# Kernel tuning notes

Measured on AMD Instinct MI355X. Metric: run time of the kernel, lower is better.

The kernel has to match this reference:

```python
import jax, jax.numpy as jnp
import numpy as np

N_U, N_F = 50000, 20000
N = N_U + N_F
U_DIM, F_DIM, HID = 64, 128, 128
E = 2_000_000        # graph edges
E_PRED = 2_000_000   # prediction pairs
EPS = 1e-5
SLOPE = 0.01         # default leaky_relu negative slope


def setup_inputs() -> dict:
    key = jax.random.key(0)
    ks = jax.random.split(key, 20)
    s = 0.02
    inp = {
        "u_feat": jax.random.normal(ks[0], (N_U, U_DIM), jnp.float32),
        "f_feat": jax.random.normal(ks[1], (N_F, F_DIM), jnp.float32),
        "edge_index": jax.random.randint(ks[2], (2, E), 0, N, jnp.int64),
        "edge_u": jax.random.randint(ks[3], (E_PRED,), 0, N_U, jnp.int64),
        "edge_f": N_U + jax.random.randint(ks[4], (E_PRED,), 0, N_F, jnp.int64),
        # learned params
        "u_W": jax.random.normal(ks[5], (U_DIM, HID), jnp.float32) * s,
        "u_b": jnp.zeros((HID,), jnp.float32),
        "f_W": jax.random.normal(ks[6], (F_DIM, HID), jnp.float32) * s,
        "f_b": jnp.zeros((HID,), jnp.float32),
        "c1_W": jax.random.normal(ks[7], (HID, HID), jnp.float32) * s,
        "c1_b": jnp.zeros((HID,), jnp.float32),
        "c2_W": jax.random.normal(ks[8], (HID, HID), jnp.float32) * s,
        "c2_b": jnp.zeros((HID,), jnp.float32),
        "n1_g": jnp.ones((HID,), jnp.float32),
        "n1_b": jnp.zeros((HID,), jnp.float32),
        "n2_g": jnp.ones((HID,), jnp.float32),
        "n2_b": jnp.zeros((HID,), jnp.float32),
        "e_W": jax.random.normal(ks[9], (2 * HID, 1), jnp.float32) * s,
        "e_b": jnp.zeros((1,), jnp.float32),
        "r_W": jax.random.normal(ks[10], (2 * HID, 1), jnp.float32) * s,
        "r_b": jnp.zeros((1,), jnp.float32),
    }
    return inp


def _layer_norm(x, g, b):
    mu = jnp.mean(x, -1, keepdims=True)
    var = jnp.mean(jnp.square(x - mu), -1, keepdims=True)
    return (x - mu) * jax.lax.rsqrt(var + EPS) * g + b


def _gcn_conv(x, W, b, src, dst, n):
    # PyG GCNConv: add self loops, symmetric deg^{-1/2} norm, aggregate at dst.
    loop = jnp.arange(n, dtype=src.dtype)
    src_f = jnp.concatenate([src, loop])
    dst_f = jnp.concatenate([dst, loop])
    deg = jax.ops.segment_sum(jnp.ones(src_f.shape, x.dtype), dst_f, num_segments=n)
    dinv = jnp.where(deg > 0, jax.lax.rsqrt(deg), 0.0)
    norm = dinv[src_f] * dinv[dst_f]                     # [E+N]
    xw = x @ W                                           # [N, H]
    agg = jax.ops.segment_sum(xw[src_f] * norm[:, None], dst_f, num_segments=n)
    return agg + b


def reference(u_feat, f_feat, edge_index, edge_u, edge_f,
              u_W, u_b, f_W, f_b, c1_W, c1_b, c2_W, c2_b,
              n1_g, n1_b, n2_g, n2_b, e_W, e_b, r_W, r_b):
    src, dst = edge_index[0], edge_index[1]
    x = jnp.concatenate([u_feat @ u_W + u_b, f_feat @ f_W + f_b], 0)  # [N, H]
    x = jax.nn.leaky_relu(_layer_norm(_gcn_conv(x, c1_W, c1_b, src, dst, N), n1_g, n1_b), SLOPE)
    # dropout is identity in eval mode
    x = jax.nn.leaky_relu(_layer_norm(_gcn_conv(x, c2_W, c2_b, src, dst, N), n2_g, n2_b), SLOPE)
    emb = jnp.concatenate([x[edge_u], x[edge_f]], -1)                 # [E_pred, 2H]
    exist = jax.nn.sigmoid((emb @ e_W + e_b)[..., 0])
    rating = 1.0 + 4.0 * jax.nn.sigmoid((emb @ r_W + r_b)[..., 0])
    return exist, rating
```

## Files before the change

### kernel.cpp

```cpp
#include <hip/hip_runtime.h>
#include <hip/hip_bf16.h>
#include <math.h>

#define HID 128
#define SLOPE 0.01f
#define LN_EPS 1e-5f
#define NB_SCAN 256
#define NT_SCAN 256
#define BSHIFT 6
#define CHUNK 8192
#define MAXBUCK 1152

typedef __attribute__((ext_vector_type(8))) short bf16x8;
typedef __attribute__((ext_vector_type(4))) float f32x4;

__device__ __forceinline__ float bf16lo(unsigned int v) {
  unsigned int b = v << 16;
  return __builtin_bit_cast(float, b);
}
__device__ __forceinline__ float bf16hi(unsigned int v) {
  unsigned int b = v & 0xFFFF0000u;
  return __builtin_bit_cast(float, b);
}
__device__ __forceinline__ unsigned int pack_bf16(float lo, float hi) {
  __hip_bfloat16 a = __float2bfloat16(lo);
  __hip_bfloat16 b = __float2bfloat16(hi);
  return (unsigned int)__builtin_bit_cast(unsigned short, a) |
         ((unsigned int)__builtin_bit_cast(unsigned short, b) << 16);
}

__global__ __launch_bounds__(256) void hist_chunk_kernel(
    const int* __restrict__ dst, int* __restrict__ cntM,
    int E, int nbuck, int nchunk) {
  __shared__ int hist[MAXBUCK];
  int c = blockIdx.x, tid = threadIdx.x;
  for (int i = tid; i < nbuck; i += 256) hist[i] = 0;
  __syncthreads();
  int beg = c * CHUNK, end = min(beg + CHUNK, E);
  for (int e = beg + tid; e < end; e += 256)
    atomicAdd(&hist[dst[e] >> BSHIFT], 1);
  __syncthreads();
  for (int b = tid; b < nbuck; b += 256)
    cntM[(size_t)b * nchunk + c] = hist[b];
}

__global__ void scan_pass1(const int* __restrict__ cnt, int* __restrict__ blocksum, int m) {
  __shared__ int ss[NT_SCAN];
  int K = (m + NB_SCAN * NT_SCAN - 1) / (NB_SCAN * NT_SCAN);
  int t = threadIdx.x, b = blockIdx.x;
  int beg = (b * NT_SCAN + t) * K;
  int end = min(beg + K, m);
  int s = 0;
  for (int i = beg; i < end; ++i) s += cnt[i];
  ss[t] = s;
  __syncthreads();
  for (int off = NT_SCAN / 2; off > 0; off >>= 1) {
    if (t < off) ss[t] += ss[t + off];
    __syncthreads();
  }
  if (t == 0) blocksum[b] = ss[0];
}

__global__ void scan_pass2(int* __restrict__ blocksum) {
  __shared__ int ss[NB_SCAN];
  int t = threadIdx.x;
  ss[t] = blocksum[t];
  __syncthreads();
  for (int off = 1; off < NB_SCAN; off <<= 1) {
    int v = (t >= off) ? ss[t - off] : 0;
    __syncthreads();
    ss[t] += v;
    __syncthreads();
  }
  blocksum[t] = (t == 0) ? 0 : ss[t - 1];
}

__global__ void scan_pass3(const int* __restrict__ cnt, const int* __restrict__ blockoff,
                           int* __restrict__ scanM, int m) {
  __shared__ int ss[NT_SCAN];
  int K = (m + NB_SCAN * NT_SCAN - 1) / (NB_SCAN * NT_SCAN);
  int t = threadIdx.x, b = blockIdx.x;
  int beg = (b * NT_SCAN + t) * K;
  int end = min(beg + K, m);
  int s = 0;
  for (int i = beg; i < end; ++i) s += cnt[i];
  ss[t] = s;
  __syncthreads();
  for (int off = 1; off < NT_SCAN; off <<= 1) {
    int v = (t >= off) ? ss[t - off] : 0;
    __syncthreads();
    ss[t] += v;
    __syncthreads();
  }
  int pre = blockoff[b] + ((t == 0) ? 0 : ss[t - 1]);
  for (int i = beg; i < end; ++i) {
    scanM[i] = pre;
    pre += cnt[i];
    if (i == m - 1) scanM[m] = pre;
  }
}

__global__ __launch_bounds__(256) void scatter_chunk_kernel(
    const int* __restrict__ src, const int* __restrict__ dst,
    const int* __restrict__ scanM, unsigned int* __restrict__ ebuf,
    int E, int nbuck, int nchunk) {
  __shared__ int cur[MAXBUCK];
  int c = blockIdx.x, tid = threadIdx.x;
  for (int b = tid; b < nbuck; b += 256)
    cur[b] = scanM[(size_t)b * nchunk + c];
  __syncthreads();
  int beg = c * CHUNK, end = min(beg + CHUNK, E);
  for (int e = beg + tid; e < end; e += 256) {
    int s = src[e], d = dst[e];
    int pos = atomicAdd(&cur[d >> BSHIFT], 1);
    ebuf[pos] = ((unsigned)s << 6) | ((unsigned)d & 63);
  }
}

__global__ __launch_bounds__(256) void deg_rowptr_kernel(
    const unsigned int* __restrict__ ebuf, const int* __restrict__ scanM,
    int* __restrict__ rowptr, float* __restrict__ dinv,
    int n, int nbuck, int nchunk, int E) {
  __shared__ int sdeg[64];
  int b = blockIdx.x, tid = threadIdx.x;
  if (tid < 64) sdeg[tid] = 0;
  __syncthreads();
  int beg = scanM[(size_t)b * nchunk], end = scanM[(size_t)(b + 1) * nchunk];
  for (int j = beg + tid; j < end; j += 256) atomicAdd(&sdeg[ebuf[j] & 63], 1);
  __syncthreads();
  if (tid < 64) {
    int deg = sdeg[tid];
    int s = deg;
#pragma unroll
    for (int off = 1; off < 64; off <<= 1) {
      int v = __shfl_up(s, off);
      if (tid >= off) s += v;
    }
    int excl = s - deg;
    int nd = (b << BSHIFT) + tid;
    if (nd < n) {
      rowptr[nd] = beg + excl;
      dinv[nd] = rsqrtf((float)(deg + 1));
    }
    if (b == nbuck - 1 && tid == 0) rowptr[n] = E;
  }
}

__global__ __launch_bounds__(256) void fill_bucket_kernel(
    const unsigned int* __restrict__ ebuf, const int* __restrict__ scanM,
    const int* __restrict__ rowptr, const float* __restrict__ dinv,
    uint2* __restrict__ ecol, int n, int nchunk) {
  __shared__ int scur[64];
  __shared__ int srow[64];
  __shared__ float sdinv[64];
  int b = blockIdx.x, tid = threadIdx.x;
  if (tid < 64) {
    scur[tid] = 0;
    int nd = (b << BSHIFT) + tid;
    srow[tid] = (nd < n) ? rowptr[nd] : 0;
    sdinv[tid] = (nd < n) ? dinv[nd] : 0.0f;
  }
  __syncthreads();
  int beg = scanM[(size_t)b * nchunk], end = scanM[(size_t)(b + 1) * nchunk];
  for (int j = beg + tid; j < end; j += 256) {
    unsigned int v = ebuf[j];
    int ndl = (int)(v & 63);
    int s = (int)(v >> 6);
    int pos = atomicAdd(&scur[ndl], 1);
    float w = dinv[s] * sdinv[ndl];
    ecol[srow[ndl] + pos] = make_uint2((unsigned)s, __builtin_bit_cast(unsigned int, w));
  }
}

__global__ void wt_pack_kernel(const float* __restrict__ W, unsigned int* __restrict__ Wt,
                               int K) {
  int idx = blockIdx.x * 256 + threadIdx.x;
  int total = 128 * (K / 2);
  if (idx >= total) return;
  int col = idx & 127;
  int k2 = idx >> 7;
  Wt[(size_t)col * (K / 2) + k2] =
      pack_bf16(W[(size_t)(2 * k2) * 128 + col], W[(size_t)(2 * k2 + 1) * 128 + col]);
}

template<int K, bool BF16OUT>
__global__ __launch_bounds__(256) void dense_mfma_kernel(
    const float* __restrict__ feat, const unsigned int* __restrict__ Wt,
    const float* __restrict__ bias,
    float* __restrict__ outf, __hip_bfloat16* __restrict__ outb, int nrows) {
  int tid = threadIdx.x;
  int wid = tid >> 6, lane = tid & 63;
  int l15 = lane & 15, lk = lane >> 4;
  int rowbase = blockIdx.x * 32 + 16 * (wid & 1);
  int colbase = 64 * (wid >> 1);

  f32x4 acc0 = {}, acc1 = {}, acc2 = {}, acc3 = {};

  int row = rowbase + l15;
  int rrow = min(row, nrows - 1);
  const float* ap0 = feat + (size_t)rrow * K + lk * 8;

#pragma unroll
  for (int kb = 0; kb < K / 32; ++kb) {
    const float* ap = ap0 + kb * 32;
    float4 a0 = *reinterpret_cast<const float4*>(ap);
    float4 a1 = *reinterpret_cast<const float4*>(ap + 4);
    float af0 = a0.x, af1 = a0.y, af2 = a0.z, af3 = a0.w;
    float af4 = a1.x, af5 = a1.y, af6 = a1.z, af7 = a1.w;
    unsigned int b0 = __builtin_bit_cast(unsigned int, af0);
    unsigned int b1 = __builtin_bit_cast(unsigned int, af1);
    unsigned int b2 = __builtin_bit_cast(unsigned int, af2);
    unsigned int b3 = __builtin_bit_cast(unsigned int, af3);
    unsigned int b4 = __builtin_bit_cast(unsigned int, af4);
    unsigned int b5 = __builtin_bit_cast(unsigned int, af5);
    unsigned int b6 = __builtin_bit_cast(unsigned int, af6);
    unsigned int b7 = __builtin_bit_cast(unsigned int, af7);
    uint4 hv;
    hv.x = (b0 >> 16) | (b1 & 0xFFFF0000u);
    hv.y = (b2 >> 16) | (b3 & 0xFFFF0000u);
    hv.z = (b4 >> 16) | (b5 & 0xFFFF0000u);
    hv.w = (b6 >> 16) | (b7 & 0xFFFF0000u);
    uint4 lv;
    {
      float h0 = __builtin_bit_cast(float, b0 & 0xFFFF0000u);
      float h1 = __builtin_bit_cast(float, b1 & 0xFFFF0000u);
      float h2 = __builtin_bit_cast(float, b2 & 0xFFFF0000u);
      float h3 = __builtin_bit_cast(float, b3 & 0xFFFF0000u);
      float h4 = __builtin_bit_cast(float, b4 & 0xFFFF0000u);
      float h5 = __builtin_bit_cast(float, b5 & 0xFFFF0000u);
      float h6 = __builtin_bit_cast(float, b6 & 0xFFFF0000u);
      float h7 = __builtin_bit_cast(float, b7 & 0xFFFF0000u);
      lv.x = pack_bf16(af0 - h0, af1 - h1);
      lv.y = pack_bf16(af2 - h2, af3 - h3);
      lv.z = pack_bf16(af4 - h4, af5 - h5);
      lv.w = pack_bf16(af6 - h6, af7 - h7);
    }
    bf16x8 ahi = __builtin_bit_cast(bf16x8, hv);
    bf16x8 alo = __builtin_bit_cast(bf16x8, lv);

    const unsigned int* wrow = Wt + (size_t)(colbase + l15) * (K / 2) + kb * 16 + lk * 4;
    bf16x8 bf0 = __builtin_bit_cast(bf16x8, *reinterpret_cast<const uint4*>(wrow));
    bf16x8 bf1 = __builtin_bit_cast(bf16x8, *reinterpret_cast<const uint4*>(wrow + 16 * (K / 2)));
    bf16x8 bf2 = __builtin_bit_cast(bf16x8, *reinterpret_cast<const uint4*>(wrow + 32 * (K / 2)));
    bf16x8 bf3 = __builtin_bit_cast(bf16x8, *reinterpret_cast<const uint4*>(wrow + 48 * (K / 2)));
    acc0 = __builtin_amdgcn_mfma_f32_16x16x32_bf16(ahi, bf0, acc0, 0, 0, 0);
    acc0 = __builtin_amdgcn_mfma_f32_16x16x32_bf16(alo, bf0, acc0, 0, 0, 0);
    acc1 = __builtin_amdgcn_mfma_f32_16x16x32_bf16(ahi, bf1, acc1, 0, 0, 0);
    acc1 = __builtin_amdgcn_mfma_f32_16x16x32_bf16(alo, bf1, acc1, 0, 0, 0);
    acc2 = __builtin_amdgcn_mfma_f32_16x16x32_bf16(ahi, bf2, acc2, 0, 0, 0);
    acc2 = __builtin_amdgcn_mfma_f32_16x16x32_bf16(alo, bf2, acc2, 0, 0, 0);
    acc3 = __builtin_amdgcn_mfma_f32_16x16x32_bf16(ahi, bf3, acc3, 0, 0, 0);
    acc3 = __builtin_amdgcn_mfma_f32_16x16x32_bf16(alo, bf3, acc3, 0, 0, 0);
  }

#pragma unroll
  for (int t = 0; t < 4; ++t) {
    int col = colbase + 16 * t + l15;
    float bv = bias ? bias[col] : 0.0f;
    f32x4 a = (t == 0) ? acc0 : (t == 1) ? acc1 : (t == 2) ? acc2 : acc3;
#pragma unroll
    for (int r = 0; r < 4; ++r) {
      int orow = rowbase + lk * 4 + r;
      if (orow < nrows) {
        float v = a[r] + bv;
        if (BF16OUT) outb[(size_t)orow * HID + col] = __float2bfloat16(v);
        else         outf[(size_t)orow * HID + col] = v;
      }
    }
  }
}

template<bool PROJ>
__global__ void gather_norm_kernel(const int* __restrict__ rowptr,
                                   const uint2* __restrict__ ecol,
                                   const uint4* __restrict__ xwb4,
                                   const float* __restrict__ dinv,
                                   const float* __restrict__ cb,
                                   const float* __restrict__ g,
                                   const float* __restrict__ b,
                                   const float* __restrict__ eW,
                                   const float* __restrict__ rW,
                                   float* __restrict__ outx,
                                   float4* __restrict__ table, int n_nodes) {
  int d = blockIdx.x * 4 + (threadIdx.x >> 6);
  if (d >= n_nodes) return;
  int lane = threadIdx.x & 63;
  int grp = lane >> 4;
  int t = lane & 15;

  float acc[8];
#pragma unroll
  for (int k = 0; k < 8; ++k) acc[k] = 0.0f;

  float wd = dinv[d];
  int beg = rowptr[d], end = rowptr[d + 1];
  for (int j = beg + grp; j < end; j += 4) {
    uint2 e = ecol[j];
    float w = __builtin_bit_cast(float, e.y);
    uint4 v = xwb4[(size_t)e.x * 16 + t];
    acc[0] = fmaf(bf16lo(v.x), w, acc[0]);
    acc[1] = fmaf(bf16hi(v.x), w, acc[1]);
    acc[2] = fmaf(bf16lo(v.y), w, acc[2]);
    acc[3] = fmaf(bf16hi(v.y), w, acc[3]);
    acc[4] = fmaf(bf16lo(v.z), w, acc[4]);
    acc[5] = fmaf(bf16hi(v.z), w, acc[5]);
    acc[6] = fmaf(bf16lo(v.w), w, acc[6]);
    acc[7] = fmaf(bf16hi(v.w), w, acc[7]);
  }
#pragma unroll
  for (int k = 0; k < 8; ++k) {
    acc[k] += __shfl_xor(acc[k], 16);
    acc[k] += __shfl_xor(acc[k], 32);
  }
  {
    float wself = wd * wd;
    uint4 v = xwb4[(size_t)d * 16 + t];
    acc[0] = fmaf(bf16lo(v.x), wself, acc[0]);
    acc[1] = fmaf(bf16hi(v.x), wself, acc[1]);
    acc[2] = fmaf(bf16lo(v.y), wself, acc[2]);
    acc[3] = fmaf(bf16hi(v.y), wself, acc[3]);
    acc[4] = fmaf(bf16lo(v.z), wself, acc[4]);
    acc[5] = fmaf(bf16hi(v.z), wself, acc[5]);
    acc[6] = fmaf(bf16lo(v.w), wself, acc[6]);
    acc[7] = fmaf(bf16hi(v.w), wself, acc[7]);
    float4 c0 = *reinterpret_cast<const float4*>(cb + 8 * t);
    float4 c1 = *reinterpret_cast<const float4*>(cb + 8 * t + 4);
    acc[0] += c0.x; acc[1] += c0.y; acc[2] += c0.z; acc[3] += c0.w;
    acc[4] += c1.x; acc[5] += c1.y; acc[6] += c1.z; acc[7] += c1.w;
  }
  float s = acc[0] + acc[1] + acc[2] + acc[3] + acc[4] + acc[5] + acc[6] + acc[7];
#pragma unroll
  for (int m = 1; m < 16; m <<= 1) s += __shfl_xor(s, m);
  float mu = s * (1.0f / HID);
  float sq = 0.0f;
#pragma unroll
  for (int k = 0; k < 8; ++k) {
    acc[k] -= mu;
    sq = fmaf(acc[k], acc[k], sq);
  }
#pragma unroll
  for (int m = 1; m < 16; m <<= 1) sq += __shfl_xor(sq, m);
  float rs = rsqrtf(sq * (1.0f / HID) + LN_EPS);
  float4 g0 = *reinterpret_cast<const float4*>(g + 8 * t);
  float4 g1 = *reinterpret_cast<const float4*>(g + 8 * t + 4);
  float4 b0 = *reinterpret_cast<const float4*>(b + 8 * t);
  float4 b1 = *reinterpret_cast<const float4*>(b + 8 * t + 4);
  float o[8];
  o[0] = acc[0] * rs * g0.x + b0.x;
  o[1] = acc[1] * rs * g0.y + b0.y;
  o[2] = acc[2] * rs * g0.z + b0.z;
  o[3] = acc[3] * rs * g0.w + b0.w;
  o[4] = acc[4] * rs * g1.x + b1.x;
  o[5] = acc[5] * rs * g1.y + b1.y;
  o[6] = acc[6] * rs * g1.z + b1.z;
  o[7] = acc[7] * rs * g1.w + b1.w;
#pragma unroll
  for (int k = 0; k < 8; ++k) o[k] = o[k] >= 0.0f ? o[k] : SLOPE * o[k];

  if (!PROJ) {
    if (grp == 0) {
      float4* op = reinterpret_cast<float4*>(outx + (size_t)d * HID + 8 * t);
      op[0] = make_float4(o[0], o[1], o[2], o[3]);
      op[1] = make_float4(o[4], o[5], o[6], o[7]);
    }
  } else {
    float4 eu0 = *reinterpret_cast<const float4*>(eW + 8 * t);
    float4 eu1 = *reinterpret_cast<const float4*>(eW + 8 * t + 4);
    float4 ef0 = *reinterpret_cast<const float4*>(eW + HID + 8 * t);
    float4 ef1 = *reinterpret_cast<const float4*>(eW + HID + 8 * t + 4);
    float4 ru0 = *reinterpret_cast<const float4*>(rW + 8 * t);
    float4 ru1 = *reinterpret_cast<const float4*>(rW + 8 * t + 4);
    float4 rf0 = *reinterpret_cast<const float4*>(rW + HID + 8 * t);
    float4 rf1 = *reinterpret_cast<const float4*>(rW + HID + 8 * t + 4);
    float pa = o[0]*eu0.x + o[1]*eu0.y + o[2]*eu0.z + o[3]*eu0.w
             + o[4]*eu1.x + o[5]*eu1.y + o[6]*eu1.z + o[7]*eu1.w;
    float pb = o[0]*ef0.x + o[1]*ef0.y + o[2]*ef0.z + o[3]*ef0.w
             + o[4]*ef1.x + o[5]*ef1.y + o[6]*ef1.z + o[7]*ef1.w;
    float pc = o[0]*ru0.x + o[1]*ru0.y + o[2]*ru0.z + o[3]*ru0.w
             + o[4]*ru1.x + o[5]*ru1.y + o[6]*ru1.z + o[7]*ru1.w;
    float pd = o[0]*rf0.x + o[1]*rf0.y + o[2]*rf0.z + o[3]*rf0.w
             + o[4]*rf1.x + o[5]*rf1.y + o[6]*rf1.z + o[7]*rf1.w;
#pragma unroll
    for (int m = 1; m < 16; m <<= 1) {
      pa += __shfl_xor(pa, m);
      pb += __shfl_xor(pb, m);
      pc += __shfl_xor(pc, m);
      pd += __shfl_xor(pd, m);
    }
    if (lane == 0) table[d] = make_float4(pa, pb, pc, pd);
  }
}

__global__ void pair_kernel(const int* __restrict__ eu, const int* __restrict__ ef,
                            const float4* __restrict__ table,
                            const float* __restrict__ eb, const float* __restrict__ rb,
                            float* __restrict__ out_exist, float* __restrict__ out_rating,
                            int Ep) {
  int i = blockIdx.x * blockDim.x + threadIdx.x;
  if (i >= Ep) return;
  float4 tu = table[eu[i]];
  float4 tf = table[ef[i]];
  float pe = tu.x + tf.y + eb[0];
  float pr = tu.z + tf.w + rb[0];
  out_exist[i]  = 1.0f / (1.0f + expf(-pe));
  out_rating[i] = 1.0f + 4.0f / (1.0f + expf(-pr));
}

extern "C" void kernel_launch(void* const* d_in, const int* in_sizes, int n_in,
                              void* d_out, int out_size, void* d_ws, size_t ws_size,
                              hipStream_t stream) {
  const float* u_feat = (const float*)d_in[0];
  const float* f_feat = (const float*)d_in[1];
  const int*   ei     = (const int*)d_in[2];
  const int*   eu     = (const int*)d_in[3];
  const int*   ef     = (const int*)d_in[4];
  const float* u_W  = (const float*)d_in[5];
  const float* u_b  = (const float*)d_in[6];
  const float* f_W  = (const float*)d_in[7];
  const float* f_b  = (const float*)d_in[8];
  const float* c1_W = (const float*)d_in[9];
  const float* c1_b = (const float*)d_in[10];
  const float* c2_W = (const float*)d_in[11];
  const float* c2_b = (const float*)d_in[12];
  const float* n1_g = (const float*)d_in[13];
  const float* n1_b = (const float*)d_in[14];
  const float* n2_g = (const float*)d_in[15];
  const float* n2_b = (const float*)d_in[16];
  const float* e_W  = (const float*)d_in[17];
  const float* e_b  = (const float*)d_in[18];
  const float* r_W  = (const float*)d_in[19];
  const float* r_b  = (const float*)d_in[20];

  int n_u = in_sizes[0] / 64;
  int n_f = in_sizes[1] / HID;
  int n   = n_u + n_f;
  int E   = in_sizes[2] / 2;
  int Ep  = in_sizes[3];
  int nbuck  = (n + (1 << BSHIFT) - 1) >> BSHIFT;
  int nchunk = (E + CHUNK - 1) / CHUNK;
  int m      = nbuck * nchunk;

  const int* src = ei;
  const int* dst = ei + E;

  float*        x      = (float*)d_ws;
  unsigned int* xwb    = (unsigned int*)(x + (size_t)n * HID);
  float4*       table  = (float4*)(xwb + (size_t)n * (HID / 2));
  unsigned int* ebuf   = (unsigned int*)(table + n);
  uint2*        ecol   = (uint2*)(ebuf + E);
  float*        dinv   = (float*)(ecol + E);
  int*          rowptr = (int*)(dinv + n);
  int*          cntM   = rowptr + n + 1;
  int*          scanM  = cntM + m;
  int*          blocksum = scanM + m + 1;
  unsigned int* wt_u   = (unsigned int*)(blocksum + NB_SCAN);
  unsigned int* wt_f   = wt_u + 128 * 32;
  unsigned int* wt_c1  = wt_f + 128 * 64;
  unsigned int* wt_c2  = wt_c1 + 128 * 64;

  wt_pack_kernel<<<(128 * 32 + 255) / 256, 256, 0, stream>>>(u_W, wt_u, 64);
  wt_pack_kernel<<<(128 * 64 + 255) / 256, 256, 0, stream>>>(f_W, wt_f, 128);
  wt_pack_kernel<<<(128 * 64 + 255) / 256, 256, 0, stream>>>(c1_W, wt_c1, 128);
  wt_pack_kernel<<<(128 * 64 + 255) / 256, 256, 0, stream>>>(c2_W, wt_c2, 128);

  hist_chunk_kernel<<<nchunk, 256, 0, stream>>>(dst, cntM, E, nbuck, nchunk);
  scan_pass1<<<NB_SCAN, NT_SCAN, 0, stream>>>(cntM, blocksum, m);
  scan_pass2<<<1, NB_SCAN, 0, stream>>>(blocksum);
  scan_pass3<<<NB_SCAN, NT_SCAN, 0, stream>>>(cntM, blocksum, scanM, m);
  scatter_chunk_kernel<<<nchunk, 256, 0, stream>>>(src, dst, scanM, ebuf, E, nbuck, nchunk);

  deg_rowptr_kernel<<<nbuck, 256, 0, stream>>>(ebuf, scanM, rowptr, dinv,
                                               n, nbuck, nchunk, E);
  fill_bucket_kernel<<<nbuck, 256, 0, stream>>>(ebuf, scanM, rowptr, dinv, ecol,
                                                n, nchunk);

  dense_mfma_kernel<64, false><<<(n_u + 31) / 32, 256, 0, stream>>>(
      u_feat, wt_u, u_b, x, nullptr, n_u);
  dense_mfma_kernel<128, false><<<(n_f + 31) / 32, 256, 0, stream>>>(
      f_feat, wt_f, f_b, x + (size_t)n_u * HID, nullptr, n_f);

  dense_mfma_kernel<128, true><<<(n + 31) / 32, 256, 0, stream>>>(
      x, wt_c1, nullptr, nullptr, (__hip_bfloat16*)xwb, n);
  gather_norm_kernel<false><<<(n + 3) / 4, 256, 0, stream>>>(
      rowptr, ecol, (const uint4*)xwb, dinv, c1_b, n1_g, n1_b,
      nullptr, nullptr, x, nullptr, n);

  dense_mfma_kernel<128, true><<<(n + 31) / 32, 256, 0, stream>>>(
      x, wt_c2, nullptr, nullptr, (__hip_bfloat16*)xwb, n);
  gather_norm_kernel<true><<<(n + 3) / 4, 256, 0, stream>>>(
      rowptr, ecol, (const uint4*)xwb, dinv, c2_b, n2_g, n2_b,
      e_W, r_W, nullptr, table, n);

  float* out_exist  = (float*)d_out;
  float* out_rating = out_exist + Ep;
  pair_kernel<<<(Ep + 255) / 256, 256, 0, stream>>>(eu, ef, table, e_b, r_b,
                                                    out_exist, out_rating, Ep);
}
```

Measured before the change: 361.8 us.

## Fold input projections into first GCN weight and unroll edge gather by two

The input projection weights are precomputed into the first conv weight (u_W·c1_W, f_W·c1_W), and the projected biases as b·c1_W. Input features then go through a single dense MFMA straight to bf16 xw, which drops one dense pass and the fp32 x write/read over all nodes. The gather loop is also unrolled by two so two neighbour rows are in flight per lane group. The composed weights are rounded to bf16 once, which slightly changes numerics, and a few tiny setup kernels are added.

```diff
diff --git a/kernel.cpp b/kernel.cpp
--- a/kernel.cpp
+++ b/kernel.cpp
@@ -170,6 +170,32 @@
     float w = dinv[s] * sdinv[ndl];
     ecol[srow[ndl] + pos] = make_uint2((unsigned)s, __builtin_bit_cast(unsigned int, w));
   }
+}
+
+__global__ void compose_pack_kernel(const float* __restrict__ A, const float* __restrict__ B,
+                                    unsigned int* __restrict__ Wt, int K) {
+  int idx = blockIdx.x * 256 + threadIdx.x;
+  int total = 128 * (K / 2);
+  if (idx >= total) return;
+  int col = idx & 127;
+  int k2 = idx >> 7;
+  float s0 = 0.0f, s1 = 0.0f;
+  const float* a0 = A + (size_t)(2 * k2) * 128;
+  const float* a1 = a0 + 128;
+  for (int m = 0; m < 128; ++m) {
+    float bm = B[(size_t)m * 128 + col];
+    s0 = fmaf(a0[m], bm, s0);
+    s1 = fmaf(a1[m], bm, s1);
+  }
+  Wt[(size_t)col * (K / 2) + k2] = pack_bf16(s0, s1);
+}
+
+__global__ void bias_comp_kernel(const float* __restrict__ bvec, const float* __restrict__ B,
+                                 float* __restrict__ out) {
+  int j = threadIdx.x;
+  float s = 0.0f;
+  for (int m = 0; m < 128; ++m) s = fmaf(bvec[m], B[(size_t)m * 128 + j], s);
+  out[j] = s;
 }
 
 __global__ void wt_pack_kernel(const float* __restrict__ W, unsigned int* __restrict__ Wt,
@@ -294,18 +320,43 @@
 
   float wd = dinv[d];
   int beg = rowptr[d], end = rowptr[d + 1];
-  for (int j = beg + grp; j < end; j += 4) {
-    uint2 e = ecol[j];
-    float w = __builtin_bit_cast(float, e.y);
-    uint4 v = xwb4[(size_t)e.x * 16 + t];
-    acc[0] = fmaf(bf16lo(v.x), w, acc[0]);
-    acc[1] = fmaf(bf16hi(v.x), w, acc[1]);
-    acc[2] = fmaf(bf16lo(v.y), w, acc[2]);
-    acc[3] = fmaf(bf16hi(v.y), w, acc[3]);
-    acc[4] = fmaf(bf16lo(v.z), w, acc[4]);
-    acc[5] = fmaf(bf16hi(v.z), w, acc[5]);
-    acc[6] = fmaf(bf16lo(v.w), w, acc[6]);
-    acc[7] = fmaf(bf16hi(v.w), w, acc[7]);
+  int j = beg + grp;
+  for (; j + 4 < end; j += 8) {
+    uint2 e0 = ecol[j];
+    uint2 e1 = ecol[j + 4];
+    uint4 v0 = xwb4[(size_t)e0.x * 16 + t];
+    uint4 v1 = xwb4[(size_t)e1.x * 16 + t];
+    float w0 = __builtin_bit_cast(float, e0.y);
+    float w1 = __builtin_bit_cast(float, e1.y);
+    acc[0] = fmaf(bf16lo(v0.x), w0, acc[0]);
+    acc[1] = fmaf(bf16hi(v0.x), w0, acc[1]);
+    acc[2] = fmaf(bf16lo(v0.y), w0, acc[2]);
+    acc[3] = fmaf(bf16hi(v0.y), w0, acc[3]);
+    acc[4] = fmaf(bf16lo(v0.z), w0, acc[4]);
+    acc[5] = fmaf(bf16hi(v0.z), w0, acc[5]);
+    acc[6] = fmaf(bf16lo(v0.w), w0, acc[6]);
+    acc[7] = fmaf(bf16hi(v0.w), w0, acc[7]);
+    acc[0] = fmaf(bf16lo(v1.x), w1, acc[0]);
+    acc[1] = fmaf(bf16hi(v1.x), w1, acc[1]);
+    acc[2] = fmaf(bf16lo(v1.y), w1, acc[2]);
+    acc[3] = fmaf(bf16hi(v1.y), w1, acc[3]);
+    acc[4] = fmaf(bf16lo(v1.z), w1, acc[4]);
+    acc[5] = fmaf(bf16hi(v1.z), w1, acc[5]);
+    acc[6] = fmaf(bf16lo(v1.w), w1, acc[6]);
+    acc[7] = fmaf(bf16hi(v1.w), w1, acc[7]);
+  }
+  if (j < end) {
+    uint2 e0 = ecol[j];
+    uint4 v0 = xwb4[(size_t)e0.x * 16 + t];
+    float w0 = __builtin_bit_cast(float, e0.y);
+    acc[0] = fmaf(bf16lo(v0.x), w0, acc[0]);
+    acc[1] = fmaf(bf16hi(v0.x), w0, acc[1]);
+    acc[2] = fmaf(bf16lo(v0.y), w0, acc[2]);
+    acc[3] = fmaf(bf16hi(v0.y), w0, acc[3]);
+    acc[4] = fmaf(bf16lo(v0.z), w0, acc[4]);
+    acc[5] = fmaf(bf16hi(v0.z), w0, acc[5]);
+    acc[6] = fmaf(bf16lo(v0.w), w0, acc[6]);
+    acc[7] = fmaf(bf16hi(v0.w), w0, acc[7]);
   }
 #pragma unroll
   for (int k = 0; k < 8; ++k) {
@@ -453,14 +504,16 @@
   int*          cntM   = rowptr + n + 1;
   int*          scanM  = cntM + m;
   int*          blocksum = scanM + m + 1;
-  unsigned int* wt_u   = (unsigned int*)(blocksum + NB_SCAN);
-  unsigned int* wt_f   = wt_u + 128 * 32;
-  unsigned int* wt_c1  = wt_f + 128 * 64;
-  unsigned int* wt_c2  = wt_c1 + 128 * 64;
-
-  wt_pack_kernel<<<(128 * 32 + 255) / 256, 256, 0, stream>>>(u_W, wt_u, 64);
-  wt_pack_kernel<<<(128 * 64 + 255) / 256, 256, 0, stream>>>(f_W, wt_f, 128);
-  wt_pack_kernel<<<(128 * 64 + 255) / 256, 256, 0, stream>>>(c1_W, wt_c1, 128);
+  unsigned int* wt_u1  = (unsigned int*)(blocksum + NB_SCAN);
+  unsigned int* wt_f1  = wt_u1 + 128 * 32;
+  unsigned int* wt_c2  = wt_f1 + 128 * 64;
+  float*        bc_u   = (float*)(wt_c2 + 128 * 64);
+  float*        bc_f   = bc_u + 128;
+
+  compose_pack_kernel<<<(128 * 32 + 255) / 256, 256, 0, stream>>>(u_W, c1_W, wt_u1, 64);
+  compose_pack_kernel<<<(128 * 64 + 255) / 256, 256, 0, stream>>>(f_W, c1_W, wt_f1, 128);
+  bias_comp_kernel<<<1, 128, 0, stream>>>(u_b, c1_W, bc_u);
+  bias_comp_kernel<<<1, 128, 0, stream>>>(f_b, c1_W, bc_f);
   wt_pack_kernel<<<(128 * 64 + 255) / 256, 256, 0, stream>>>(c2_W, wt_c2, 128);
 
   hist_chunk_kernel<<<nchunk, 256, 0, stream>>>(dst, cntM, E, nbuck, nchunk);
@@ -474,13 +527,10 @@
   fill_bucket_kernel<<<nbuck, 256, 0, stream>>>(ebuf, scanM, rowptr, dinv, ecol,
                                                 n, nchunk);
 
-  dense_mfma_kernel<64, false><<<(n_u + 31) / 32, 256, 0, stream>>>(
-      u_feat, wt_u, u_b, x, nullptr, n_u);
-  dense_mfma_kernel<128, false><<<(n_f + 31) / 32, 256, 0, stream>>>(
-      f_feat, wt_f, f_b, x + (size_t)n_u * HID, nullptr, n_f);
-
-  dense_mfma_kernel<128, true><<<(n + 31) / 32, 256, 0, stream>>>(
-      x, wt_c1, nullptr, nullptr, (__hip_bfloat16*)xwb, n);
+  dense_mfma_kernel<64, true><<<(n_u + 31) / 32, 256, 0, stream>>>(
+      u_feat, wt_u1, bc_u, nullptr, (__hip_bfloat16*)xwb, n_u);
+  dense_mfma_kernel<128, true><<<(n_f + 31) / 32, 256, 0, stream>>>(
+      f_feat, wt_f1, bc_f, nullptr, ((__hip_bfloat16*)xwb) + (size_t)n_u * HID, n_f);
   gather_norm_kernel<false><<<(n + 3) / 4, 256, 0, stream>>>(
       rowptr, ecol, (const uint4*)xwb, dinv, c1_b, n1_g, n1_b,
       nullptr, nullptr, x, nullptr, n);
```

Result: faster. 325.0 us (-10.2%).
